# Kernel tuning notes

Measured on AMD Instinct MI355X. Metric: run time of the kernel, lower is better.

The kernel has to match this reference:

```python
import jax, jax.numpy as jnp
import numpy as np

DIM = 512
EPS = 1e-8
LN_EPS = 1e-5


def _layernorm(x, g, b):
    mu = jnp.mean(x, axis=-1, keepdims=True)
    var = jnp.mean(jnp.square(x - mu), axis=-1, keepdims=True)
    return (x - mu) * jax.lax.rsqrt(var + LN_EPS) * g + b


def setup_inputs() -> dict:
    key = jax.random.key(0)
    ks = jax.random.split(key, 8)
    b, i, j, d = 8, 2048, 2048, DIM
    s = 1.0 / np.sqrt(d)
    return {
        "inputs": jax.random.normal(ks[0], (b, i, d), dtype=jnp.float32),
        "context": jax.random.normal(ks[1], (b, j, d), dtype=jnp.float32),
        "g_in": jnp.ones((d,), jnp.float32),
        "b_in": jnp.zeros((d,), jnp.float32),
        "g_ctx": jnp.ones((d,), jnp.float32),
        "b_ctx": jnp.zeros((d,), jnp.float32),
        "Wq": jax.random.uniform(ks[2], (d, d), jnp.float32, -s, s),
        "bq": jnp.zeros((d,), jnp.float32),
        "Wk": jax.random.uniform(ks[3], (d, d), jnp.float32, -s, s),
        "bk": jnp.zeros((d,), jnp.float32),
        "Wv": jax.random.uniform(ks[4], (d, d), jnp.float32, -s, s),
        "bv": jnp.zeros((d,), jnp.float32),
    }


def reference(inputs, context, g_in, b_in, g_ctx, b_ctx, Wq, bq, Wk, bk, Wv, bv):
    scale = DIM ** (-0.5)
    x = _layernorm(inputs, g_in, b_in)
    c = _layernorm(context, g_ctx, b_ctx)
    q = x @ Wq + bq          # [b,i,d]
    k = c @ Wk + bk          # [b,j,d]
    v = c @ Wv + bv          # [b,j,d]
    dots = jnp.einsum('bid,bjd->bij', q, k) * scale
    # NOTE: non-standard softmax over the QUERY axis (dim=1), then eps shift
    attn = jax.nn.softmax(dots, axis=1) + EPS
    # second renormalization over the KEY axis (dim=2)
    mean_attn = attn / (jnp.sum(attn, axis=2, keepdims=True) + EPS)
    updates = jnp.einsum('bjd,bij->bid', v, mean_attn)
    return updates
```

## Files before the change

kernel.cpp:

```cpp
#include <hip/hip_runtime.h>
#include <hip/hip_bf16.h>
#include <math.h>

#define EPSF 1e-8f
#define LN_EPSF 1e-5f
#define SCALE_QK 0.04419417382415922f

typedef unsigned short ushort_t;
typedef __bf16 bhalf;
typedef bhalf bhalf8 __attribute__((ext_vector_type(8)));
typedef float f32x4 __attribute__((ext_vector_type(4)));

__device__ __forceinline__ float b2f(ushort_t u) {
    return __uint_as_float((unsigned)u << 16);
}
__device__ __forceinline__ ushort_t f2b(float f) {
    unsigned x = __float_as_uint(f);
    return (ushort_t)((x + 0x7fffu + ((x >> 16) & 1u)) >> 16);
}
__device__ __forceinline__ unsigned pk2(float lo, float hi) {
    return (unsigned)f2b(lo) | ((unsigned)f2b(hi) << 16);
}
__device__ __forceinline__ void gload16(const ushort_t* g, ushort_t* l) {
    __builtin_amdgcn_global_load_lds(
        (const __attribute__((address_space(1))) unsigned int*)g,
        (__attribute__((address_space(3))) unsigned int*)l, 16, 0, 0);
}

__global__ __launch_bounds__(256) void mv_bias_kernel(
    const float* __restrict__ Wq, const float* __restrict__ Wk,
    const float* __restrict__ bq, const float* __restrict__ bk,
    float* __restrict__ wqbk, float* __restrict__ wkbq, float* __restrict__ cc)
{
    __shared__ float ls[4];
    const int y = blockIdx.y;
    const int t = threadIdx.x;
    if (y == 2) {
        if (blockIdx.x != 0) return;
        float s = bq[t] * bk[t] + bq[t + 256] * bk[t + 256];
#pragma unroll
        for (int off = 32; off > 0; off >>= 1) s += __shfl_down(s, off, 64);
        int lane = t & 63, w = t >> 6;
        if (lane == 0) ls[w] = s;
        __syncthreads();
        if (t == 0) cc[0] = ls[0] + ls[1] + ls[2] + ls[3];
        return;
    }
    const float* W = y ? Wk : Wq;
    const float* v = y ? bq : bk;
    float* o = y ? wkbq : wqbk;
    const int row = blockIdx.x * 16 + (t >> 4);
    const int l = t & 15;
    const float* wr = W + (size_t)row * 512 + l * 32;
    const float* vr = v + l * 32;
    float s = 0.f;
#pragma unroll
    for (int c = 0; c < 32; ++c) s += wr[c] * vr[c];
#pragma unroll
    for (int off = 8; off > 0; off >>= 1) s += __shfl_down(s, off, 16);
    if (l == 0) o[row] = s;
}

__global__ __launch_bounds__(256) void ln_apply_kernel(
    const float* __restrict__ X1, const float* __restrict__ X2,
    const float* __restrict__ g1, const float* __restrict__ b1,
    const float* __restrict__ g2, const float* __restrict__ b2,
    const float* __restrict__ wb1, const float* __restrict__ wb2,
    ushort_t* __restrict__ O1, ushort_t* __restrict__ O2,
    float* __restrict__ T1, float* __restrict__ T2)
{
    const bool sec = blockIdx.y != 0;
    const float* X = sec ? X2 : X1;
    const float* g = sec ? g2 : g1;
    const float* b = sec ? b2 : b1;
    const float* wb = sec ? wb2 : wb1;
    ushort_t* O = sec ? O2 : O1;
    float* T = sec ? T2 : T1;
    const size_t base = (size_t)blockIdx.x * 512;
    const int t = threadIdx.x;
    float2 x = ((const float2*)(X + base))[t];
    float s = x.x + x.y;
    float q = fmaf(x.x, x.x, x.y * x.y);
#pragma unroll
    for (int off = 32; off > 0; off >>= 1) {
        s += __shfl_down(s, off, 64);
        q += __shfl_down(q, off, 64);
    }
    __shared__ float ls[4], lq[4], mv[2], ld[4];
    int lane = t & 63, w = t >> 6;
    if (lane == 0) { ls[w] = s; lq[w] = q; }
    __syncthreads();
    if (t == 0) {
        float st = ls[0] + ls[1] + ls[2] + ls[3];
        float qt = lq[0] + lq[1] + lq[2] + lq[3];
        float mu = st * (1.0f / 512.0f);
        float var = qt * (1.0f / 512.0f) - mu * mu;
        mv[0] = mu;
        mv[1] = rsqrtf(var + LN_EPSF);
    }
    __syncthreads();
    const float mu = mv[0], rstd = mv[1];
    float2 gg = ((const float2*)g)[t];
    float2 bb = ((const float2*)b)[t];
    float2 ww = ((const float2*)wb)[t];
    float o0 = (x.x - mu) * rstd * gg.x + bb.x;
    float o1 = (x.y - mu) * rstd * gg.y + bb.y;
    ((unsigned*)O)[blockIdx.x * 256 + t] = pk2(o0, o1);
    float d = o0 * ww.x + o1 * ww.y;
#pragma unroll
    for (int off = 32; off > 0; off >>= 1) d += __shfl_down(d, off, 64);
    if (lane == 0) ld[w] = d;
    __syncthreads();
    if (t == 0) T[blockIdx.x] = ld[0] + ld[1] + ld[2] + ld[3];
}

__global__ __launch_bounds__(256) void wprep_kernel(
    const float* __restrict__ Wq, const float* __restrict__ Wk,
    const float* __restrict__ Wv,
    ushort_t* __restrict__ Wqb, ushort_t* __restrict__ Wkb,
    ushort_t* __restrict__ WvT)
{
    const int z = blockIdx.z;
    if (z < 2) {
        const float* W = z ? Wk : Wq;
        ushort_t* T = z ? Wkb : Wqb;
        size_t idx = ((size_t)(blockIdx.y * 16 + blockIdx.x)) * 1024 + threadIdx.x * 4;
        float4 f = *(const float4*)(W + idx);
        uint2 u;
        u.x = pk2(f.x, f.y);
        u.y = pk2(f.z, f.w);
        *(uint2*)(T + idx) = u;
        return;
    }
    __shared__ float tile[32][33];
    int tx = threadIdx.x & 31, ty = threadIdx.x >> 5;
    int r0 = blockIdx.y * 32, c0 = blockIdx.x * 32;
#pragma unroll
    for (int p = 0; p < 4; ++p)
        tile[ty + p * 8][tx] = Wv[(size_t)(r0 + ty + p * 8) * 512 + c0 + tx];
    __syncthreads();
#pragma unroll
    for (int p = 0; p < 4; ++p)
        WvT[(size_t)(c0 + ty + p * 8) * 512 + r0 + tx] = f2b(tile[tx][ty + p * 8]);
}

__global__ __launch_bounds__(256) void colrecip_kernel(
    const float* __restrict__ cs, float* __restrict__ cr,
    ushort_t* __restrict__ crs)
{
    int t = blockIdx.x * 256 + threadIdx.x;
    float r = 1.0f / cs[t];
    cr[t] = r;
    crs[t] = f2b(r);
}

__global__ __launch_bounds__(512) void gemm256_exp_kernel(
    const ushort_t* __restrict__ A, const ushort_t* __restrict__ B,
    ushort_t* __restrict__ Cout,
    const float* __restrict__ t1, const float* __restrict__ t2,
    const float* __restrict__ cc, float* __restrict__ colsum,
    int K, int N, size_t strideA, size_t strideB, size_t strideC,
    float scale)
{
    __shared__ __align__(16) ushort_t As0[256 * 64];
    __shared__ __align__(16) ushort_t As1[256 * 64];
    __shared__ __align__(16) ushort_t Bs0[256 * 64];
    __shared__ __align__(16) ushort_t Bs1[256 * 64];
    const int tid = threadIdx.x;

    const int nbx = gridDim.x, nby = gridDim.y;
    const int nwg = nbx * nby * gridDim.z;
    int lin = blockIdx.x + nbx * (blockIdx.y + nby * blockIdx.z);
    int swz = (lin & 7) * (nwg >> 3) + (lin >> 3);
    const int sx = __builtin_ctz(nbx), sy = __builtin_ctz(nby);
    const int bx = swz & (nbx - 1);
    const int by = (swz >> sx) & (nby - 1);
    const int bz = swz >> (sx + sy);

    const ushort_t* Ab = A + strideA * bz;
    const ushort_t* Bb = B + strideB * bz;
    const int m0 = by * 256;
    const int n0 = bx * 256;
    const int wave = tid >> 6;
    const int lane = tid & 63;
    const int fm = lane & 15;
    const int fq = lane >> 4;
    const int fq4 = fq * 4;
    const int wm = (wave >> 2) * 128;
    const int wn = (wave & 3) * 64;

    const int lrow = lane >> 3;
    const int lchunk = lane & 7;
    const int scs = lchunk ^ lrow;

    const ushort_t* aSrc[4]; const ushort_t* bSrc[4];
#pragma unroll
    for (int p = 0; p < 4; ++p) {
        int row = wave * 32 + p * 8 + lrow;
        aSrc[p] = Ab + (size_t)(m0 + row) * K + scs * 8;
        bSrc[p] = Bb + (size_t)(n0 + row) * K + scs * 8;
    }
    const int dOff = wave * 2048 + lane * 8;

    const int cBase = fq ^ (fm & 7);

    f32x4 acc[8][4];
#pragma unroll
    for (int i = 0; i < 8; ++i)
#pragma unroll
        for (int j = 0; j < 4; ++j) acc[i][j] = (f32x4){0.f, 0.f, 0.f, 0.f};

    auto stage = [&](ushort_t* Ad, ushort_t* Bd, int k0) {
#pragma unroll
        for (int p = 0; p < 4; ++p) {
            gload16(aSrc[p] + k0, Ad + dOff + p * 512);
            gload16(bSrc[p] + k0, Bd + dOff + p * 512);
        }
    };
    auto compute = [&](const ushort_t* Asb, const ushort_t* Bsb) {
#pragma unroll
        for (int s = 0; s < 2; ++s) {
            const int off = ((cBase ^ (s << 2)) << 3);
            bhalf8 af[8], bfr[4];
#pragma unroll
            for (int u = 0; u < 8; ++u)
                af[u] = *(const bhalf8*)(Asb + (wm + u * 16 + fm) * 64 + off);
#pragma unroll
            for (int u = 0; u < 4; ++u)
                bfr[u] = *(const bhalf8*)(Bsb + (wn + u * 16 + fm) * 64 + off);
#pragma unroll
            for (int i = 0; i < 8; ++i)
#pragma unroll
                for (int j = 0; j < 4; ++j)
                    acc[i][j] = __builtin_amdgcn_mfma_f32_16x16x32_bf16(
                        bfr[j], af[i], acc[i][j], 0, 0, 0);
        }
    };

#define WAITV8  { asm volatile("s_waitcnt vmcnt(8)" ::: "memory"); \
                  __builtin_amdgcn_sched_barrier(0); }
#define WAITV0  { asm volatile("s_waitcnt vmcnt(0)" ::: "memory"); \
                  __builtin_amdgcn_sched_barrier(0); }
#define FENCE_LGKM { asm volatile("s_waitcnt lgkmcnt(0)" ::: "memory"); \
                     __builtin_amdgcn_sched_barrier(0); }

    const int nk = K >> 6;
    stage(As0, Bs0, 0);
    stage(As1, Bs1, 64);
    for (int t = 0; t < nk - 2; t += 2) {
        WAITV8;
        __builtin_amdgcn_s_barrier();
        compute(As0, Bs0);
        FENCE_LGKM;
        __builtin_amdgcn_s_barrier();
        stage(As0, Bs0, (t + 2) << 6);
        WAITV8;
        __builtin_amdgcn_s_barrier();
        compute(As1, Bs1);
        FENCE_LGKM;
        __builtin_amdgcn_s_barrier();
        stage(As1, Bs1, (t + 3) << 6);
    }
    WAITV8;
    __builtin_amdgcn_s_barrier();
    compute(As0, Bs0);
    WAITV0;
    __builtin_amdgcn_s_barrier();
    compute(As1, Bs1);
#undef WAITV8
#undef WAITV0
#undef FENCE_LGKM

    ushort_t* C = Cout + strideC * bz;
    const float cv = cc[0];
    f32x4 t2c[4];
#pragma unroll
    for (int nj = 0; nj < 4; ++nj) {
        float4 tv = *(const float4*)(t2 + (size_t)bz * 2048 +
                                     n0 + wn + nj * 16 + fq4);
        t2c[nj][0] = tv.x + cv;
        t2c[nj][1] = tv.y + cv;
        t2c[nj][2] = tv.z + cv;
        t2c[nj][3] = tv.w + cv;
    }
    float psum[4][4];
#pragma unroll
    for (int nj = 0; nj < 4; ++nj)
#pragma unroll
        for (int r = 0; r < 4; ++r) psum[nj][r] = 0.f;
#pragma unroll
    for (int mi = 0; mi < 8; ++mi) {
        const int row = m0 + wm + mi * 16 + fm;
        const float t1v = t1[(size_t)bz * 2048 + row];
        ushort_t* Cr = C + (size_t)row * N + n0 + wn + fq4;
#pragma unroll
        for (int nj = 0; nj < 4; ++nj) {
            ushort_t h0 = f2b(__expf((acc[mi][nj][0] + t1v + t2c[nj][0]) * scale));
            ushort_t h1 = f2b(__expf((acc[mi][nj][1] + t1v + t2c[nj][1]) * scale));
            ushort_t h2 = f2b(__expf((acc[mi][nj][2] + t1v + t2c[nj][2]) * scale));
            ushort_t h3 = f2b(__expf((acc[mi][nj][3] + t1v + t2c[nj][3]) * scale));
            uint2 u;
            u.x = (unsigned)h0 | ((unsigned)h1 << 16);
            u.y = (unsigned)h2 | ((unsigned)h3 << 16);
            *(uint2*)(Cr + nj * 16) = u;
            psum[nj][0] += b2f(h0);
            psum[nj][1] += b2f(h1);
            psum[nj][2] += b2f(h2);
            psum[nj][3] += b2f(h3);
        }
    }
#pragma unroll
    for (int nj = 0; nj < 4; ++nj)
#pragma unroll
        for (int r = 0; r < 4; ++r) {
            float v = psum[nj][r];
            v += __shfl_xor(v, 1, 64);
            v += __shfl_xor(v, 2, 64);
            v += __shfl_xor(v, 4, 64);
            v += __shfl_xor(v, 8, 64);
            psum[nj][r] = v;
        }
    float* colpart = (float*)&As0[0];
    __syncthreads();
    if (tid < 256) colpart[tid] = 0.f;
    __syncthreads();
    if (fm == 0) {
#pragma unroll
        for (int nj = 0; nj < 4; ++nj)
#pragma unroll
            for (int r = 0; r < 4; ++r)
                atomicAdd(&colpart[wn + nj * 16 + fq4 + r], psum[nj][r]);
    }
    __syncthreads();
    if (tid < 256)
        atomicAdd(&colsum[(size_t)bz * 2048 + n0 + tid], colpart[tid]);
}

template <int MODE>
__global__ __launch_bounds__(256) void mfma_gemm_kernel(
    const ushort_t* __restrict__ A, const ushort_t* __restrict__ B,
    void* __restrict__ Cout,
    const float* __restrict__ bias,
    const float* __restrict__ crcol,
    const ushort_t* __restrict__ crs,
    int K, int N, size_t strideA, size_t strideB, size_t strideC)
{
    __shared__ __align__(16) ushort_t As[128 * 64];
    __shared__ __align__(16) ushort_t Bs[128 * 64];
    __shared__ __align__(16) ushort_t crs_lds[(MODE == 2) ? 2048 : 8];
    const int tid = threadIdx.x;

    const int nbx = gridDim.x, nby = gridDim.y, nbz = gridDim.z;
    const int nwg = nbx * nby * nbz;
    int bx, by, bz;
    if ((nwg & 7) == 0) {
        int lin = blockIdx.x + nbx * (blockIdx.y + nby * blockIdx.z);
        int swz = (lin & 7) * (nwg >> 3) + (lin >> 3);
        const int sx = __builtin_ctz(nbx), sy = __builtin_ctz(nby);
        bx = swz & (nbx - 1);
        by = (swz >> sx) & (nby - 1);
        bz = swz >> (sx + sy);
    } else {
        bx = blockIdx.x; by = blockIdx.y; bz = blockIdx.z;
    }

    const ushort_t* Ab = A + strideA * bz;
    const ushort_t* Bb = B + strideB * bz;
    const int m0 = by * 128;
    const int n0 = bx * 128;
    const int wave = tid >> 6;
    const int lane = tid & 63;
    const int fm = lane & 15;
    const int fq = lane >> 4;
    const int fq4 = fq * 4;
    const int fm7 = fm & 7;
    const int wm = (wave >> 1) * 64;
    const int wn = (wave & 1) * 64;

    const int lrow = lane >> 3;
    const int lchunk = lane & 7;
    const int scs = lchunk ^ lrow;

    const ushort_t* aSrc[4]; const ushort_t* bSrc[4];
    ushort_t* aDst[4]; ushort_t* bDst[4];
#pragma unroll
    for (int p = 0; p < 4; ++p) {
        int row = wave * 32 + p * 8 + lrow;
        aSrc[p] = Ab + (size_t)(m0 + row) * K + scs * 8;
        bSrc[p] = Bb + (size_t)(n0 + row) * K + scs * 8;
        aDst[p] = As + (wave * 32 + p * 8) * 64 + lane * 8;
        bDst[p] = Bs + (wave * 32 + p * 8) * 64 + lane * 8;
    }

    if (MODE == 2) {
        uint4 c4 = *(const uint4*)(crs + (size_t)bz * 2048 + tid * 8);
        *(uint4*)&crs_lds[tid * 8] = c4;
    }

    const int cBase = fq ^ fm7;
    const ushort_t* aFrag[4]; const ushort_t* bFrag[4];
#pragma unroll
    for (int t = 0; t < 4; ++t) {
        aFrag[t] = As + (wm + t * 16 + fm) * 64;
        bFrag[t] = Bs + (wn + t * 16 + fm) * 64;
    }

    f32x4 acc[4][4];
    f32x4 sacc[4];
#pragma unroll
    for (int i = 0; i < 4; ++i) {
        sacc[i] = (f32x4){0.f, 0.f, 0.f, 0.f};
#pragma unroll
        for (int j = 0; j < 4; ++j) acc[i][j] = (f32x4){0.f, 0.f, 0.f, 0.f};
    }

    for (int k0 = 0; k0 < K; k0 += 64) {
        __syncthreads();
#pragma unroll
        for (int p = 0; p < 4; ++p) {
            gload16(aSrc[p] + k0, aDst[p]);
            gload16(bSrc[p] + k0, bDst[p]);
        }
        __syncthreads();
#pragma unroll
        for (int s = 0; s < 2; ++s) {
            const int off = ((cBase ^ (s << 2)) << 3);
            bhalf8 af[4], bfr[4];
#pragma unroll
            for (int u = 0; u < 4; ++u) {
                af[u]  = *(const bhalf8*)(aFrag[u] + off);
                bfr[u] = *(const bhalf8*)(bFrag[u] + off);
            }
#pragma unroll
            for (int i = 0; i < 4; ++i)
#pragma unroll
                for (int j = 0; j < 4; ++j)
                    acc[i][j] = __builtin_amdgcn_mfma_f32_16x16x32_bf16(
                        bfr[j], af[i], acc[i][j], 0, 0, 0);
            if (MODE == 2) {
                bhalf8 bc = *(const bhalf8*)&crs_lds[k0 + (s << 5) + (fq << 3)];
#pragma unroll
                for (int i = 0; i < 4; ++i)
                    sacc[i] = __builtin_amdgcn_mfma_f32_16x16x32_bf16(
                        bc, af[i], sacc[i], 0, 0, 0);
            }
        }
    }

    if (MODE == 2) {
        float* C = (float*)Cout + strideC * bz;
#pragma unroll
        for (int ti = 0; ti < 4; ++ti) {
            const int row = m0 + wm + ti * 16 + fm;
            const float rs = 1.0f / (sacc[ti][0] + 2.049e-5f);
            float* Cr = C + (size_t)row * N + n0 + wn + fq4;
#pragma unroll
            for (int tj = 0; tj < 4; ++tj) {
                f32x4 v;
#pragma unroll
                for (int r = 0; r < 4; ++r) v[r] = acc[ti][tj][r] * rs;
                *(f32x4*)(Cr + tj * 16) = v;
            }
        }
    } else if (MODE == 3) {
        ushort_t* C = (ushort_t*)Cout + strideC * bz;
        f32x4 crv[4];
#pragma unroll
        for (int tj = 0; tj < 4; ++tj) {
            float4 cq = *(const float4*)(crcol + (size_t)bz * 2048 +
                                         n0 + wn + tj * 16 + fq4);
            crv[tj][0] = cq.x; crv[tj][1] = cq.y;
            crv[tj][2] = cq.z; crv[tj][3] = cq.w;
        }
#pragma unroll
        for (int ti = 0; ti < 4; ++ti) {
            const int row = m0 + wm + ti * 16 + fm;
            const float bvv = bias[row];
            ushort_t* Cr = C + (size_t)row * N + n0 + wn + fq4;
#pragma unroll
            for (int tj = 0; tj < 4; ++tj) {
                uint2 u;
                u.x = pk2((acc[ti][tj][0] + bvv) * crv[tj][0],
                          (acc[ti][tj][1] + bvv) * crv[tj][1]);
                u.y = pk2((acc[ti][tj][2] + bvv) * crv[tj][2],
                          (acc[ti][tj][3] + bvv) * crv[tj][3]);
                *(uint2*)(Cr + tj * 16) = u;
            }
        }
    } else {
        ushort_t* C = (ushort_t*)Cout + strideC * bz;
#pragma unroll
        for (int ti = 0; ti < 4; ++ti) {
            const int row = m0 + wm + ti * 16 + fm;
            ushort_t* Cr = C + (size_t)row * N + n0 + wn + fq4;
#pragma unroll
            for (int tj = 0; tj < 4; ++tj) {
                uint2 u;
                u.x = pk2(acc[ti][tj][0], acc[ti][tj][1]);
                u.y = pk2(acc[ti][tj][2], acc[ti][tj][3]);
                *(uint2*)(Cr + tj * 16) = u;
            }
        }
    }
}

extern "C" void kernel_launch(void* const* d_in, const int* in_sizes, int n_in,
                              void* d_out, int out_size, void* d_ws, size_t ws_size,
                              hipStream_t stream)
{
    const float* inputs  = (const float*)d_in[0];
    const float* context = (const float*)d_in[1];
    const float* g_in    = (const float*)d_in[2];
    const float* b_in    = (const float*)d_in[3];
    const float* g_ctx   = (const float*)d_in[4];
    const float* b_ctx   = (const float*)d_in[5];
    const float* Wq      = (const float*)d_in[6];
    const float* bq      = (const float*)d_in[7];
    const float* Wk      = (const float*)d_in[8];
    const float* bk      = (const float*)d_in[9];
    const float* Wv      = (const float*)d_in[10];
    const float* bv      = (const float*)d_in[11];
    float* out = (float*)d_out;

    const size_t QKV  = 8ull * 2048 * 512;
    const size_t WSZ  = 512ull * 512;
    const size_t DOTS = 8ull * 2048 * 2048;

    ushort_t* xln   = (ushort_t*)d_ws;
    ushort_t* cln   = xln + QKV;
    ushort_t* Wqb   = cln + QKV;
    ushort_t* Wkb   = Wqb + WSZ;
    ushort_t* WvT   = Wkb + WSZ;
    ushort_t* Mb    = WvT + WSZ;
    ushort_t* KM    = Mb + WSZ;
    ushort_t* vTs   = KM + QKV;
    ushort_t* edots = vTs + QKV;
    ushort_t* crs   = edots + DOTS;
    float* fbase    = (float*)(crs + 16384);
    float* colsum   = fbase;
    float* colrecip = colsum + 16384;
    float* t1       = colrecip + 16384;
    float* t2       = t1 + 16384;
    float* wqbk     = t2 + 16384;
    float* wkbq     = wqbk + 512;
    float* cc       = wkbq + 512;
    size_t need_bytes = (4 * QKV + 4 * WSZ + DOTS + 16384) * 2
                      + (4 * 16384 + 1024 + 1) * 4;
    if (ws_size < need_bytes) return;

    hipMemsetAsync(colsum, 0, 16384 * sizeof(float), stream);

    mv_bias_kernel<<<dim3(32, 3), 256, 0, stream>>>(Wq, Wk, bq, bk, wqbk, wkbq, cc);

    ln_apply_kernel<<<dim3(16384, 2), 256, 0, stream>>>(
        inputs, context, g_in, b_in, g_ctx, b_ctx, wqbk, wkbq, xln, cln, t1, t2);

    wprep_kernel<<<dim3(16, 16, 3), 256, 0, stream>>>(Wq, Wk, Wv, Wqb, Wkb, WvT);

    mfma_gemm_kernel<0><<<dim3(4, 4, 1), 256, 0, stream>>>(
        Wqb, Wkb, Mb, nullptr, nullptr, nullptr,
        512, 512, 0, 0, 0);

    mfma_gemm_kernel<0><<<dim3(4, 128, 1), 256, 0, stream>>>(
        cln, Mb, KM, nullptr, nullptr, nullptr,
        512, 512, 0, 0, 0);

    gemm256_exp_kernel<<<dim3(8, 8, 8), 512, 0, stream>>>(
        xln, KM, edots, t1, t2, cc, colsum,
        512, 2048, (size_t)2048 * 512, (size_t)2048 * 512, (size_t)2048 * 2048,
        SCALE_QK);

    colrecip_kernel<<<64, 256, 0, stream>>>(colsum, colrecip, crs);

    mfma_gemm_kernel<3><<<dim3(16, 4, 8), 256, 0, stream>>>(
        WvT, cln, vTs, bv, colrecip, nullptr,
        512, 2048, 0, (size_t)2048 * 512, (size_t)512 * 2048);

    mfma_gemm_kernel<2><<<dim3(4, 16, 8), 256, 0, stream>>>(
        edots, vTs, out, nullptr, nullptr, crs,
        2048, 512, (size_t)2048 * 2048, (size_t)512 * 2048, (size_t)2048 * 512);
}
```

Baseline: 303.4 us.

## Replace output GEMM with 256x128 double-buffered async-load kernel

The final attention-times-V GEMM (K=2048) moves from the generic 128x128 single-buffered kernel to a dedicated 512-thread kernel with 256x128 tiles. It double-buffers LDS and uses vmcnt-based waits so global-to-LDS loads overlap MFMA compute, the same scheme the exp GEMM already uses. The row-sum MFMA and the reciprocal scaling move into the new kernel, and the MODE 2 path is removed from the template. The larger tile halves the block count and raises LDS use to about 100KB, which limits occupancy.

```diff
diff --git a/kernel.cpp b/kernel.cpp
--- a/kernel.cpp
+++ b/kernel.cpp
@@ -26,6 +26,11 @@
         (const __attribute__((address_space(1))) unsigned int*)g,
         (__attribute__((address_space(3))) unsigned int*)l, 16, 0, 0);
 }
+
+#define WAITV(N) { asm volatile("s_waitcnt vmcnt(" #N ")" ::: "memory"); \
+                   __builtin_amdgcn_sched_barrier(0); }
+#define FENCE_LGKM { asm volatile("s_waitcnt lgkmcnt(0)" ::: "memory"); \
+                     __builtin_amdgcn_sched_barrier(0); }
 
 __global__ __launch_bounds__(256) void mv_bias_kernel(
     const float* __restrict__ Wq, const float* __restrict__ Wk,
@@ -237,39 +242,29 @@
         }
     };
 
-#define WAITV8  { asm volatile("s_waitcnt vmcnt(8)" ::: "memory"); \
-                  __builtin_amdgcn_sched_barrier(0); }
-#define WAITV0  { asm volatile("s_waitcnt vmcnt(0)" ::: "memory"); \
-                  __builtin_amdgcn_sched_barrier(0); }
-#define FENCE_LGKM { asm volatile("s_waitcnt lgkmcnt(0)" ::: "memory"); \
-                     __builtin_amdgcn_sched_barrier(0); }
-
     const int nk = K >> 6;
     stage(As0, Bs0, 0);
     stage(As1, Bs1, 64);
     for (int t = 0; t < nk - 2; t += 2) {
-        WAITV8;
+        WAITV(8);
         __builtin_amdgcn_s_barrier();
         compute(As0, Bs0);
         FENCE_LGKM;
         __builtin_amdgcn_s_barrier();
         stage(As0, Bs0, (t + 2) << 6);
-        WAITV8;
+        WAITV(8);
         __builtin_amdgcn_s_barrier();
         compute(As1, Bs1);
         FENCE_LGKM;
         __builtin_amdgcn_s_barrier();
         stage(As1, Bs1, (t + 3) << 6);
     }
-    WAITV8;
+    WAITV(8);
     __builtin_amdgcn_s_barrier();
     compute(As0, Bs0);
-    WAITV0;
+    WAITV(0);
     __builtin_amdgcn_s_barrier();
     compute(As1, Bs1);
-#undef WAITV8
-#undef WAITV0
-#undef FENCE_LGKM
 
     ushort_t* C = Cout + strideC * bz;
     const float cv = cc[0];
@@ -336,18 +331,156 @@
         atomicAdd(&colsum[(size_t)bz * 2048 + n0 + tid], colpart[tid]);
 }
 
+__global__ __launch_bounds__(512) void gemm_out256_kernel(
+    const ushort_t* __restrict__ A, const ushort_t* __restrict__ B,
+    float* __restrict__ Cout, const ushort_t* __restrict__ crs,
+    int K, int N, size_t strideA, size_t strideB, size_t strideC)
+{
+    __shared__ __align__(16) ushort_t As0[256 * 64];
+    __shared__ __align__(16) ushort_t As1[256 * 64];
+    __shared__ __align__(16) ushort_t Bs0[128 * 64];
+    __shared__ __align__(16) ushort_t Bs1[128 * 64];
+    __shared__ __align__(16) ushort_t crs_lds[2048];
+    const int tid = threadIdx.x;
+
+    const int nbx = gridDim.x, nby = gridDim.y;
+    const int nwg = nbx * nby * gridDim.z;
+    int lin = blockIdx.x + nbx * (blockIdx.y + nby * blockIdx.z);
+    int swz = (lin & 7) * (nwg >> 3) + (lin >> 3);
+    const int sx = __builtin_ctz(nbx), sy = __builtin_ctz(nby);
+    const int bx = swz & (nbx - 1);
+    const int by = (swz >> sx) & (nby - 1);
+    const int bz = swz >> (sx + sy);
+
+    const ushort_t* Ab = A + strideA * bz;
+    const ushort_t* Bb = B + strideB * bz;
+    const int m0 = by * 256;
+    const int n0 = bx * 128;
+    const int wave = tid >> 6;
+    const int lane = tid & 63;
+    const int fm = lane & 15;
+    const int fq = lane >> 4;
+    const int fq4 = fq * 4;
+    const int wm = (wave >> 1) * 64;
+    const int wn = (wave & 1) * 64;
+
+    const int lrow = lane >> 3;
+    const int lchunk = lane & 7;
+    const int scs = lchunk ^ lrow;
+
+    const ushort_t* aSrc[4]; const ushort_t* bSrc[2];
+#pragma unroll
+    for (int p = 0; p < 4; ++p) {
+        int row = wave * 32 + p * 8 + lrow;
+        aSrc[p] = Ab + (size_t)(m0 + row) * K + scs * 8;
+    }
+#pragma unroll
+    for (int p = 0; p < 2; ++p) {
+        int row = wave * 16 + p * 8 + lrow;
+        bSrc[p] = Bb + (size_t)(n0 + row) * K + scs * 8;
+    }
+    const int aOff = wave * 2048 + lane * 8;
+    const int bOff = wave * 1024 + lane * 8;
+
+    if (tid < 256) {
+        uint4 c4 = *(const uint4*)(crs + (size_t)bz * 2048 + tid * 8);
+        *(uint4*)&crs_lds[tid * 8] = c4;
+    }
+    __syncthreads();
+
+    const int cBase = fq ^ (fm & 7);
+
+    f32x4 acc[4][4];
+    f32x4 sacc[4];
+#pragma unroll
+    for (int i = 0; i < 4; ++i) {
+        sacc[i] = (f32x4){0.f, 0.f, 0.f, 0.f};
+#pragma unroll
+        for (int j = 0; j < 4; ++j) acc[i][j] = (f32x4){0.f, 0.f, 0.f, 0.f};
+    }
+
+    auto stage = [&](ushort_t* Ad, ushort_t* Bd, int k0) {
+#pragma unroll
+        for (int p = 0; p < 4; ++p)
+            gload16(aSrc[p] + k0, Ad + aOff + p * 512);
+#pragma unroll
+        for (int p = 0; p < 2; ++p)
+            gload16(bSrc[p] + k0, Bd + bOff + p * 512);
+    };
+    auto compute = [&](const ushort_t* Asb, const ushort_t* Bsb, int k0) {
+#pragma unroll
+        for (int s = 0; s < 2; ++s) {
+            const int off = ((cBase ^ (s << 2)) << 3);
+            bhalf8 af[4], bfr[4];
+#pragma unroll
+            for (int u = 0; u < 4; ++u) {
+                af[u]  = *(const bhalf8*)(Asb + (wm + u * 16 + fm) * 64 + off);
+                bfr[u] = *(const bhalf8*)(Bsb + (wn + u * 16 + fm) * 64 + off);
+            }
+#pragma unroll
+            for (int i = 0; i < 4; ++i)
+#pragma unroll
+                for (int j = 0; j < 4; ++j)
+                    acc[i][j] = __builtin_amdgcn_mfma_f32_16x16x32_bf16(
+                        bfr[j], af[i], acc[i][j], 0, 0, 0);
+            bhalf8 bc = *(const bhalf8*)&crs_lds[k0 + (s << 5) + (fq << 3)];
+#pragma unroll
+            for (int i = 0; i < 4; ++i)
+                sacc[i] = __builtin_amdgcn_mfma_f32_16x16x32_bf16(
+                    bc, af[i], sacc[i], 0, 0, 0);
+        }
+    };
+
+    const int nk = K >> 6;
+    stage(As0, Bs0, 0);
+    stage(As1, Bs1, 64);
+    for (int t = 0; t < nk - 2; t += 2) {
+        WAITV(6);
+        __builtin_amdgcn_s_barrier();
+        compute(As0, Bs0, t << 6);
+        FENCE_LGKM;
+        __builtin_amdgcn_s_barrier();
+        stage(As0, Bs0, (t + 2) << 6);
+        WAITV(6);
+        __builtin_amdgcn_s_barrier();
+        compute(As1, Bs1, (t + 1) << 6);
+        FENCE_LGKM;
+        __builtin_amdgcn_s_barrier();
+        stage(As1, Bs1, (t + 3) << 6);
+    }
+    WAITV(6);
+    __builtin_amdgcn_s_barrier();
+    compute(As0, Bs0, (nk - 2) << 6);
+    WAITV(0);
+    __builtin_amdgcn_s_barrier();
+    compute(As1, Bs1, (nk - 1) << 6);
+
+    float* C = Cout + strideC * bz;
+#pragma unroll
+    for (int ti = 0; ti < 4; ++ti) {
+        const int row = m0 + wm + ti * 16 + fm;
+        const float rs = 1.0f / (sacc[ti][0] + 2.049e-5f);
+        float* Cr = C + (size_t)row * N + n0 + wn + fq4;
+#pragma unroll
+        for (int tj = 0; tj < 4; ++tj) {
+            f32x4 v;
+#pragma unroll
+            for (int r = 0; r < 4; ++r) v[r] = acc[ti][tj][r] * rs;
+            *(f32x4*)(Cr + tj * 16) = v;
+        }
+    }
+}
+
 template <int MODE>
 __global__ __launch_bounds__(256) void mfma_gemm_kernel(
     const ushort_t* __restrict__ A, const ushort_t* __restrict__ B,
     void* __restrict__ Cout,
     const float* __restrict__ bias,
     const float* __restrict__ crcol,
-    const ushort_t* __restrict__ crs,
     int K, int N, size_t strideA, size_t strideB, size_t strideC)
 {
     __shared__ __align__(16) ushort_t As[128 * 64];
     __shared__ __align__(16) ushort_t Bs[128 * 64];
-    __shared__ __align__(16) ushort_t crs_lds[(MODE == 2) ? 2048 : 8];
     const int tid = threadIdx.x;
 
     const int nbx = gridDim.x, nby = gridDim.y, nbz = gridDim.z;
@@ -392,11 +525,6 @@
         bDst[p] = Bs + (wave * 32 + p * 8) * 64 + lane * 8;
     }
 
-    if (MODE == 2) {
-        uint4 c4 = *(const uint4*)(crs + (size_t)bz * 2048 + tid * 8);
-        *(uint4*)&crs_lds[tid * 8] = c4;
-    }
-
     const int cBase = fq ^ fm7;
     const ushort_t* aFrag[4]; const ushort_t* bFrag[4];
 #pragma unroll
@@ -406,13 +534,10 @@
     }
 
     f32x4 acc[4][4];
-    f32x4 sacc[4];
-#pragma unroll
-    for (int i = 0; i < 4; ++i) {
-        sacc[i] = (f32x4){0.f, 0.f, 0.f, 0.f};
+#pragma unroll
+    for (int i = 0; i < 4; ++i)
 #pragma unroll
         for (int j = 0; j < 4; ++j) acc[i][j] = (f32x4){0.f, 0.f, 0.f, 0.f};
-    }
 
     for (int k0 = 0; k0 < K; k0 += 64) {
         __syncthreads();
@@ -437,32 +562,10 @@
                 for (int j = 0; j < 4; ++j)
                     acc[i][j] = __builtin_amdgcn_mfma_f32_16x16x32_bf16(
                         bfr[j], af[i], acc[i][j], 0, 0, 0);
-            if (MODE == 2) {
-                bhalf8 bc = *(const bhalf8*)&crs_lds[k0 + (s << 5) + (fq << 3)];
-#pragma unroll
-                for (int i = 0; i < 4; ++i)
-                    sacc[i] = __builtin_amdgcn_mfma_f32_16x16x32_bf16(
-                        bc, af[i], sacc[i], 0, 0, 0);
-            }
-        }
-    }
-
-    if (MODE == 2) {
-        float* C = (float*)Cout + strideC * bz;
-#pragma unroll
-        for (int ti = 0; ti < 4; ++ti) {
-            const int row = m0 + wm + ti * 16 + fm;
-            const float rs = 1.0f / (sacc[ti][0] + 2.049e-5f);
-            float* Cr = C + (size_t)row * N + n0 + wn + fq4;
-#pragma unroll
-            for (int tj = 0; tj < 4; ++tj) {
-                f32x4 v;
-#pragma unroll
-                for (int r = 0; r < 4; ++r) v[r] = acc[ti][tj][r] * rs;
-                *(f32x4*)(Cr + tj * 16) = v;
-            }
-        }
-    } else if (MODE == 3) {
+        }
+    }
+
+    if (MODE == 3) {
         ushort_t* C = (ushort_t*)Cout + strideC * bz;
         f32x4 crv[4];
 #pragma unroll
@@ -558,11 +661,11 @@
     wprep_kernel<<<dim3(16, 16, 3), 256, 0, stream>>>(Wq, Wk, Wv, Wqb, Wkb, WvT);
 
     mfma_gemm_kernel<0><<<dim3(4, 4, 1), 256, 0, stream>>>(
-        Wqb, Wkb, Mb, nullptr, nullptr, nullptr,
+        Wqb, Wkb, Mb, nullptr, nullptr,
         512, 512, 0, 0, 0);
 
     mfma_gemm_kernel<0><<<dim3(4, 128, 1), 256, 0, stream>>>(
-        cln, Mb, KM, nullptr, nullptr, nullptr,
+        cln, Mb, KM, nullptr, nullptr,
         512, 512, 0, 0, 0);
 
     gemm256_exp_kernel<<<dim3(8, 8, 8), 512, 0, stream>>>(
@@ -573,10 +676,10 @@
     colrecip_kernel<<<64, 256, 0, stream>>>(colsum, colrecip, crs);
 
     mfma_gemm_kernel<3><<<dim3(16, 4, 8), 256, 0, stream>>>(
-        WvT, cln, vTs, bv, colrecip, nullptr,
+        WvT, cln, vTs, bv, colrecip,
         512, 2048, 0, (size_t)2048 * 512, (size_t)512 * 2048);
 
-    mfma_gemm_kernel<2><<<dim3(4, 16, 8), 256, 0, stream>>>(
-        edots, vTs, out, nullptr, nullptr, crs,
+    gemm_out256_kernel<<<dim3(4, 8, 8), 512, 0, stream>>>(
+        edots, vTs, out, crs,
         2048, 512, (size_t)2048 * 2048, (size_t)512 * 2048, (size_t)2048 * 512);
 }
```

Result: no change. 298.8 us (-1.5%).
